# Optimization experiments

Hardware: AMD Instinct MI355X
Metric: run time of the kernel (lower is better)

## Reference

```python
import jax, jax.numpy as jnp
import numpy as np

BSZ, IN_DIM, HID, OUT_DIM, N_ITERS = 262144, 64, 128, 64, 30


def setup_inputs() -> dict:
    key = jax.random.key(0)
    ks = jax.random.split(key, 6)
    s_h = 1.0 / np.sqrt(HID)
    s_i = 1.0 / np.sqrt(IN_DIM)
    return {
        "x": jax.random.normal(ks[0], (BSZ, IN_DIM), dtype=jnp.float32),
        "Wz": jax.random.uniform(ks[1], (HID, HID), jnp.float32, -s_h, s_h) * 0.9,  # scaled for contraction
        "Ux": jax.random.uniform(ks[2], (HID, IN_DIM), jnp.float32, -s_i, s_i),
        "b": jax.random.uniform(ks[3], (HID,), jnp.float32, -s_h, s_h),
        "Wd": jax.random.uniform(ks[4], (OUT_DIM, HID), jnp.float32, -s_h, s_h),
        "bd": jax.random.uniform(ks[5], (OUT_DIM,), jnp.float32, -s_h, s_h),
        "n_iters": N_ITERS,
    }


def reference(x, Wz, Ux, b, Wd, bd, n_iters):
    # injection term is iteration-invariant: compute once
    inj = x @ Ux.T + b                     # [B, HID]
    z0 = jnp.zeros((x.shape[0], Wz.shape[0]), dtype=x.dtype)

    def step(z, _):
        z = jax.nn.relu(z @ Wz.T + inj)    # f(z, x)
        return z, None

    z_star, _ = jax.lax.scan(step, z0, None, length=n_iters)
    return z_star @ Wd.T + bd              # decoder Linear
```

## Files before the change

### kernel.cpp

```cpp
#include <hip/hip_runtime.h>


typedef __attribute__((ext_vector_type(8))) __bf16 bf16x8;
typedef __attribute__((ext_vector_type(4))) __bf16 bf16x4;
typedef __attribute__((ext_vector_type(4))) float  floatx4;

#define MFMA16(a, b, c) __builtin_amdgcn_mfma_f32_16x16x32_bf16((a), (b), (c), 0, 0, 0)

static constexpr int kBsz = 262144;
static constexpr int kTM  = 32;

__device__ __forceinline__ bf16x8 cvt_bf16x8(float4 a, float4 b) {
  bf16x8 r;
  r[0] = (__bf16)a.x; r[1] = (__bf16)a.y; r[2] = (__bf16)a.z; r[3] = (__bf16)a.w;
  r[4] = (__bf16)b.x; r[5] = (__bf16)b.y; r[6] = (__bf16)b.z; r[7] = (__bf16)b.w;
  return r;
}

__global__ void __launch_bounds__(128) deq_fused(
    const float* __restrict__ x,
    const float* __restrict__ Wz,
    const float* __restrict__ Ux,
    const float* __restrict__ bvec,
    const float* __restrict__ Wd,
    const float* __restrict__ bd,
    const int*  __restrict__ n_iters_p,
    float* __restrict__ out)
{
  __shared__ __align__(16) __bf16 zl[2][kTM][136];

  const int tid  = threadIdx.x;
  const int lane = tid & 63;
  const int wn   = tid >> 6;
  const int l15  = lane & 15;
  const int quad = lane >> 4;
  const int row0 = blockIdx.x * kTM;
  const int iters = *n_iters_p;

  bf16x8 awz[4][4];
#pragma unroll
  for (int nt = 0; nt < 4; ++nt) {
    const int n = 64 * wn + 16 * nt + l15;
#pragma unroll
    for (int ks = 0; ks < 4; ++ks) {
      const float4* p = (const float4*)(Wz + n * 128 + 32 * ks + 8 * quad);
      awz[nt][ks] = cvt_bf16x8(p[0], p[1]);
    }
  }

  floatx4 inj[4][2];
#pragma unroll
  for (int nt = 0; nt < 4; ++nt) {
    const float4 bv = *(const float4*)(bvec + 64 * wn + 16 * nt + 4 * quad);
#pragma unroll
    for (int mt = 0; mt < 2; ++mt) {
      floatx4 v = {bv.x, bv.y, bv.z, bv.w};
      inj[nt][mt] = v;
    }
  }
  {
    bf16x8 aux[4][2];
#pragma unroll
    for (int nt = 0; nt < 4; ++nt) {
      const int n = 64 * wn + 16 * nt + l15;
#pragma unroll
      for (int ks = 0; ks < 2; ++ks) {
        const float4* p = (const float4*)(Ux + n * 64 + 32 * ks + 8 * quad);
        aux[nt][ks] = cvt_bf16x8(p[0], p[1]);
      }
    }
#pragma unroll
    for (int mt = 0; mt < 2; ++mt) {
      const int m = row0 + 16 * mt + l15;
#pragma unroll
      for (int ks = 0; ks < 2; ++ks) {
        const float4* p = (const float4*)(x + m * 64 + 32 * ks + 8 * quad);
        const bf16x8 bx = cvt_bf16x8(p[0], p[1]);
#pragma unroll
        for (int nt = 0; nt < 4; ++nt)
          inj[nt][mt] = MFMA16(aux[nt][ks], bx, inj[nt][mt]);
      }
    }
  }

#pragma unroll
  for (int mt = 0; mt < 2; ++mt) {
    const int ml = 16 * mt + l15;
#pragma unroll
    for (int nt = 0; nt < 4; ++nt) {
      bf16x4 z4;
#pragma unroll
      for (int i = 0; i < 4; ++i) z4[i] = (__bf16)fmaxf(inj[nt][mt][i], 0.0f);
      *(bf16x4*)&zl[0][ml][64 * wn + 16 * nt + 4 * quad] = z4;
    }
  }

  int pb = 0;
  for (int t = 0; t < iters - 1; ++t) {
    __syncthreads();
    bf16x8 bz[2][4];
#pragma unroll
    for (int mt = 0; mt < 2; ++mt) {
      const int ml = 16 * mt + l15;
#pragma unroll
      for (int ks = 0; ks < 4; ++ks)
        bz[mt][ks] = *(const bf16x8*)&zl[pb][ml][32 * ks + 8 * quad];
    }
    const int nb = pb ^ 1;
#pragma unroll
    for (int mt = 0; mt < 2; ++mt) {
      const int ml = 16 * mt + l15;
#pragma unroll
      for (int nt = 0; nt < 4; ++nt) {
        floatx4 acc = inj[nt][mt];
#pragma unroll
        for (int ks = 0; ks < 4; ++ks)
          acc = MFMA16(awz[nt][ks], bz[mt][ks], acc);
        bf16x4 z4;
#pragma unroll
        for (int i = 0; i < 4; ++i) z4[i] = (__bf16)fmaxf(acc[i], 0.0f);
        *(bf16x4*)&zl[nb][ml][64 * wn + 16 * nt + 4 * quad] = z4;
      }
    }
    pb = nb;
  }
  __syncthreads();

  bf16x8 awd[2][4];
#pragma unroll
  for (int ot = 0; ot < 2; ++ot) {
    const int o = 32 * wn + 16 * ot + l15;
#pragma unroll
    for (int ks = 0; ks < 4; ++ks) {
      const float4* p = (const float4*)(Wd + o * 128 + 32 * ks + 8 * quad);
      awd[ot][ks] = cvt_bf16x8(p[0], p[1]);
    }
  }
#pragma unroll
  for (int mt = 0; mt < 2; ++mt) {
    const int ml = 16 * mt + l15;
    bf16x8 bz[4];
#pragma unroll
    for (int ks = 0; ks < 4; ++ks)
      bz[ks] = *(const bf16x8*)&zl[pb][ml][32 * ks + 8 * quad];
#pragma unroll
    for (int ot = 0; ot < 2; ++ot) {
      const float4 bv = *(const float4*)(bd + 32 * wn + 16 * ot + 4 * quad);
      floatx4 acc = {bv.x, bv.y, bv.z, bv.w};
#pragma unroll
      for (int ks = 0; ks < 4; ++ks)
        acc = MFMA16(awd[ot][ks], bz[ks], acc);
      float4 ov;
      ov.x = acc[0]; ov.y = acc[1]; ov.z = acc[2]; ov.w = acc[3];
      *(float4*)(out + (size_t)(row0 + ml) * 64 + 32 * wn + 16 * ot + 4 * quad) = ov;
    }
  }
}

extern "C" void kernel_launch(void* const* d_in, const int* in_sizes, int n_in,
                              void* d_out, int out_size, void* d_ws, size_t ws_size,
                              hipStream_t stream) {
  const float* x  = (const float*)d_in[0];
  const float* Wz = (const float*)d_in[1];
  const float* Ux = (const float*)d_in[2];
  const float* b  = (const float*)d_in[3];
  const float* Wd = (const float*)d_in[4];
  const float* bd = (const float*)d_in[5];
  const int* n_it = (const int*)d_in[6];
  float* outp = (float*)d_out;
  (void)in_sizes; (void)n_in; (void)d_ws; (void)ws_size; (void)out_size;

  dim3 grid(kBsz / kTM);
  deq_fused<<<grid, 128, 0, stream>>>(x, Wz, Ux, b, Wd, bd, n_it, outp);
}
```

Before: 357.8 us.

## Split row tiles across four waves per block instead of two

Doubles the block to 256 threads so each wave owns one 16-row M tile and one 64-column N half, instead of two M tiles. This halves per-wave MFMA work per iteration and per-wave accumulator/B-fragment registers, so more waves are resident and latency is hidden better. The trade-off is that each block still loads the full Wz fragments per wave (duplicated weight registers across more waves) and there are more waves synchronizing at each barrier.

```diff
diff --git a/kernel.cpp b/kernel.cpp
--- a/kernel.cpp
+++ b/kernel.cpp
@@ -17,7 +17,7 @@
   return r;
 }
 
-__global__ void __launch_bounds__(128) deq_fused(
+__global__ void __launch_bounds__(256, 4) deq_fused(
     const float* __restrict__ x,
     const float* __restrict__ Wz,
     const float* __restrict__ Ux,
@@ -31,10 +31,13 @@
 
   const int tid  = threadIdx.x;
   const int lane = tid & 63;
-  const int wn   = tid >> 6;
+  const int wv   = tid >> 6;
+  const int wn   = wv & 1;
+  const int wm   = wv >> 1;
   const int l15  = lane & 15;
   const int quad = lane >> 4;
   const int row0 = blockIdx.x * kTM;
+  const int ml   = 16 * wm + l15;
   const int iters = *n_iters_p;
 
   bf16x8 awz[4][4];
@@ -48,79 +51,58 @@
     }
   }
 
-  floatx4 inj[4][2];
+  floatx4 inj[4];
 #pragma unroll
   for (int nt = 0; nt < 4; ++nt) {
     const float4 bv = *(const float4*)(bvec + 64 * wn + 16 * nt + 4 * quad);
-#pragma unroll
-    for (int mt = 0; mt < 2; ++mt) {
-      floatx4 v = {bv.x, bv.y, bv.z, bv.w};
-      inj[nt][mt] = v;
-    }
+    floatx4 v = {bv.x, bv.y, bv.z, bv.w};
+    inj[nt] = v;
   }
   {
-    bf16x8 aux[4][2];
+    bf16x8 bx[2];
+#pragma unroll
+    for (int ks = 0; ks < 2; ++ks) {
+      const float4* p = (const float4*)(x + (size_t)(row0 + ml) * 64 + 32 * ks + 8 * quad);
+      bx[ks] = cvt_bf16x8(p[0], p[1]);
+    }
 #pragma unroll
     for (int nt = 0; nt < 4; ++nt) {
       const int n = 64 * wn + 16 * nt + l15;
 #pragma unroll
       for (int ks = 0; ks < 2; ++ks) {
         const float4* p = (const float4*)(Ux + n * 64 + 32 * ks + 8 * quad);
-        aux[nt][ks] = cvt_bf16x8(p[0], p[1]);
-      }
-    }
-#pragma unroll
-    for (int mt = 0; mt < 2; ++mt) {
-      const int m = row0 + 16 * mt + l15;
-#pragma unroll
-      for (int ks = 0; ks < 2; ++ks) {
-        const float4* p = (const float4*)(x + m * 64 + 32 * ks + 8 * quad);
-        const bf16x8 bx = cvt_bf16x8(p[0], p[1]);
-#pragma unroll
-        for (int nt = 0; nt < 4; ++nt)
-          inj[nt][mt] = MFMA16(aux[nt][ks], bx, inj[nt][mt]);
+        const bf16x8 a = cvt_bf16x8(p[0], p[1]);
+        inj[nt] = MFMA16(a, bx[ks], inj[nt]);
       }
     }
   }
 
 #pragma unroll
-  for (int mt = 0; mt < 2; ++mt) {
-    const int ml = 16 * mt + l15;
+  for (int nt = 0; nt < 4; ++nt) {
+    bf16x4 z4;
 #pragma unroll
-    for (int nt = 0; nt < 4; ++nt) {
-      bf16x4 z4;
-#pragma unroll
-      for (int i = 0; i < 4; ++i) z4[i] = (__bf16)fmaxf(inj[nt][mt][i], 0.0f);
-      *(bf16x4*)&zl[0][ml][64 * wn + 16 * nt + 4 * quad] = z4;
-    }
+    for (int i = 0; i < 4; ++i) z4[i] = (__bf16)fmaxf(inj[nt][i], 0.0f);
+    *(bf16x4*)&zl[0][ml][64 * wn + 16 * nt + 4 * quad] = z4;
   }
 
   int pb = 0;
   for (int t = 0; t < iters - 1; ++t) {
     __syncthreads();
-    bf16x8 bz[2][4];
+    bf16x8 bz[4];
 #pragma unroll
-    for (int mt = 0; mt < 2; ++mt) {
-      const int ml = 16 * mt + l15;
+    for (int ks = 0; ks < 4; ++ks)
+      bz[ks] = *(const bf16x8*)&zl[pb][ml][32 * ks + 8 * quad];
+    const int nb = pb ^ 1;
+#pragma unroll
+    for (int nt = 0; nt < 4; ++nt) {
+      floatx4 acc = inj[nt];
 #pragma unroll
       for (int ks = 0; ks < 4; ++ks)
-        bz[mt][ks] = *(const bf16x8*)&zl[pb][ml][32 * ks + 8 * quad];
-    }
-    const int nb = pb ^ 1;
+        acc = MFMA16(awz[nt][ks], bz[ks], acc);
+      bf16x4 z4;
 #pragma unroll
-    for (int mt = 0; mt < 2; ++mt) {
-      const int ml = 16 * mt + l15;
-#pragma unroll
-      for (int nt = 0; nt < 4; ++nt) {
-        floatx4 acc = inj[nt][mt];
-#pragma unroll
-        for (int ks = 0; ks < 4; ++ks)
-          acc = MFMA16(awz[nt][ks], bz[mt][ks], acc);
-        bf16x4 z4;
-#pragma unroll
-        for (int i = 0; i < 4; ++i) z4[i] = (__bf16)fmaxf(acc[i], 0.0f);
-        *(bf16x4*)&zl[nb][ml][64 * wn + 16 * nt + 4 * quad] = z4;
-      }
+      for (int i = 0; i < 4; ++i) z4[i] = (__bf16)fmaxf(acc[i], 0.0f);
+      *(bf16x4*)&zl[nb][ml][64 * wn + 16 * nt + 4 * quad] = z4;
     }
     pb = nb;
   }
@@ -136,9 +118,7 @@
       awd[ot][ks] = cvt_bf16x8(p[0], p[1]);
     }
   }
-#pragma unroll
-  for (int mt = 0; mt < 2; ++mt) {
-    const int ml = 16 * mt + l15;
+  {
     bf16x8 bz[4];
 #pragma unroll
     for (int ks = 0; ks < 4; ++ks)
@@ -171,5 +151,5 @@
   (void)in_sizes; (void)n_in; (void)d_ws; (void)ws_size; (void)out_size;
 
   dim3 grid(kBsz / kTM);
-  deq_fused<<<grid, 128, 0, stream>>>(x, Wz, Ux, b, Wd, bd, n_it, outp);
+  deq_fused<<<grid, 256, 0, stream>>>(x, Wz, Ux, b, Wd, bd, n_it, outp);
 }
```

Result: slower. 378.9 us (+5.9%).
